# Kernel optimization log

Measured on AMD Instinct MI355X. Metric: run time of the kernel, lower is better.

## Reference

```python
import jax, jax.numpy as jnp
import numpy as np

EPS = 1e-12  # matches torch F.normalize eps

def _l2norm(v, axis):
    n = jnp.sqrt(jnp.sum(v * v, axis=axis, keepdims=True))
    return v / jnp.maximum(n, EPS)

def setup_inputs() -> dict:
    key = jax.random.key(0)
    k1, k2, k3 = jax.random.split(key, 3)
    N, D, H, W, K = 64, 128, 56, 56, 64
    x = jax.random.normal(k1, (N, D, H, W), dtype=jnp.float32)
    conv_w = jax.random.normal(k2, (K, D), dtype=jnp.float32) * 0.05
    centroids = jax.random.uniform(k3, (K, D), dtype=jnp.float32)
    return {"x": x, "conv_w": conv_w, "centroids": centroids}

def reference(x, conv_w, centroids):
    # x: [N, D, H, W]; conv_w: [K, D] (1x1 conv, no bias); centroids: [K, D]
    N, D, H, W = x.shape
    K = centroids.shape[0]
    L = H * W
    # descriptor-wise L2 normalization over channel dim
    x = _l2norm(x, axis=1)
    xf = x.reshape(N, D, L)                      # [N, D, L]
    # 1x1 conv == per-pixel matmul; softmax over clusters
    logits = jnp.einsum('ndl,kd->nkl', xf, conv_w)  # [N, K, L]
    a = jax.nn.softmax(logits, axis=1)              # [N, K, L]
    # vlad[n,k,d] = sum_l a[n,k,l] * (x[n,d,l] - c[k,d])
    #            = (a @ x^T) - (sum_l a) * c   (matmul reformulation)
    vlad = jnp.einsum('nkl,ndl->nkd', a, xf) - a.sum(axis=-1)[:, :, None] * centroids[None]
    # intra-normalize over descriptor dim, flatten, global L2 normalize
    vlad = _l2norm(vlad, axis=2)
    vlad = vlad.reshape(N, K * D)
    vlad = _l2norm(vlad, axis=1)
    return vlad
```

## Files before the change

### kernel.cpp

```cpp
#include <hip/hip_runtime.h>
#include <hip/hip_bf16.h>

#define N_   64
#define D_   128
#define L_   3136
#define K_   64
#define TL_  64
#define NG_  12
#define ASH  72

typedef short  short8  __attribute__((ext_vector_type(8)));
typedef short  short4v __attribute__((ext_vector_type(4)));
typedef float  f32x16  __attribute__((ext_vector_type(16)));

static __device__ __forceinline__ unsigned short f2bf(float f) {
    unsigned u = __float_as_uint(f);
    return (unsigned short)((u + 0x7FFFu + ((u >> 16) & 1u)) >> 16);
}
static __device__ __forceinline__ float bf2f(short s) {
    return __uint_as_float(((unsigned)(unsigned short)s) << 16);
}
static __device__ __forceinline__ unsigned pk2(float lo, float hi) {
    __hip_bfloat162 b = __float22bfloat162_rn(make_float2(lo, hi));
    return *reinterpret_cast<unsigned*>(&b);
}

#define BARX() asm volatile("s_waitcnt lgkmcnt(0)\n\ts_barrier" ::: "memory")

__global__ __launch_bounds__(256, 2)
void vlad_main(const float* __restrict__ x, const float* __restrict__ w,
               float* __restrict__ vout, float* __restrict__ aout,
               int vstride, int astride)
{
    __shared__ __align__(16) short L1[TL_ * D_];
    __shared__ __align__(16) short L2[D_ * TL_];
    __shared__ __align__(16) char  AsRaw[K_ * ASH * 2];
    __shared__ float nrm_lds[TL_];
    __shared__ float dred[4][32];

    const int t    = threadIdx.x;
    const int lane = t & 63;
    const int wv   = __builtin_amdgcn_readfirstlane(t >> 6);
    const int n    = blockIdx.x / NG_;
    const int g    = blockIdx.x % NG_;
    const int tile0 = (g == 0) ? 0 : (4 * g + 1);
    const int ntile = (g == 0) ? 5 : 4;

    const int Mt = wv & 1;
    const int lg = lane >> 5;
    const int lm = lane & 31;

    char* L1b = (char*)L1;
    char* L2b = (char*)L2;
    short* AsS = (short*)AsRaw;
    float (*red_ss)[68] = (float (*)[68])AsRaw;

    short8 wf[8];
#pragma unroll
    for (int ks = 0; ks < 8; ++ks) {
        const float* wp = w + (size_t)(32 * Mt + lm) * D_ + 16 * ks + 8 * lg;
        const float4 wa = *(const float4*)wp;
        const float4 wb = *(const float4*)(wp + 4);
        union { unsigned u[4]; short8 s; } f;
        f.u[0] = pk2(wa.x, wa.y); f.u[1] = pk2(wa.z, wa.w);
        f.u[2] = pk2(wb.x, wb.y); f.u[3] = pk2(wb.z, wb.w);
        wf[ks] = f.s;
    }

    f32x16 acc0 = {0};
    f32x16 acc1 = {0};
    float asum_acc = 0.f;

    const int q  = t >> 4;
    const int l0 = (t & 15) * 4;
    const float* xb = x + (size_t)n * D_ * L_;

    float4 v[8];
    {
        const int p0 = tile0 * TL_;
#pragma unroll
        for (int r = 0; r < 8; ++r)
            v[r] = *(const float4*)(xb + (size_t)(8 * q + r) * L_ + p0 + l0);
    }

    for (int ti = 0; ti < ntile; ++ti) {
#pragma unroll
        for (int j = 0; j < 4; ++j) {
            float s = 0.f;
#pragma unroll
            for (int r = 0; r < 8; ++r) {
                const float val = (&v[r].x)[j];
                s = fmaf(val, val, s);
            }
            red_ss[q][l0 + j] = s;
        }
#pragma unroll
        for (int j = 0; j < 4; ++j) {
            const int l = l0 + j;
            union { unsigned u[4]; short8 s; } f;
            f.u[0] = pk2((&v[0].x)[j], (&v[1].x)[j]);
            f.u[1] = pk2((&v[2].x)[j], (&v[3].x)[j]);
            f.u[2] = pk2((&v[4].x)[j], (&v[5].x)[j]);
            f.u[3] = pk2((&v[6].x)[j], (&v[7].x)[j]);
            *(short8*)(L1b + l * 256 + ((16 * q) ^ ((l & 15) << 4))) = f.s;
        }
#pragma unroll
        for (int r = 0; r < 8; ++r) {
            const int d = 8 * q + r;
            union { unsigned u[2]; short4v s; } f;
            f.u[0] = pk2(v[r].x, v[r].y);
            f.u[1] = pk2(v[r].z, v[r].w);
            *(short4v*)(L2b + d * 128 + ((l0 * 2) ^ ((d & 7) << 4))) = f.s;
        }
        if (ti + 1 < ntile) {
            const int p0n = (tile0 + ti + 1) * TL_;
#pragma unroll
            for (int r = 0; r < 8; ++r)
                v[r] = *(const float4*)(xb + (size_t)(8 * q + r) * L_ + p0n + l0);
        }
        BARX();
        if (t < TL_) {
            float ss = 0.f;
#pragma unroll
            for (int qq = 0; qq < 16; ++qq) ss += red_ss[qq][t];
            nrm_lds[t] = fmaxf(sqrtf(ss), 1e-12f);
        }
        f32x16 r1 = {0};
        {
            const int l = 32 * (wv >> 1) + lm;
            const int rowoff = l * 256;
            const int swz = (l & 15) << 4;
            __builtin_amdgcn_s_setprio(1);
#pragma unroll
            for (int ks = 0; ks < 8; ++ks) {
                const short8 bfr = *(short8*)(L1b + rowoff + (((16 * ks + 8 * lg) * 2) ^ swz));
                r1 = __builtin_amdgcn_mfma_f32_32x32x16_bf16(wf[ks], bfr, r1, 0, 0, 0);
            }
            __builtin_amdgcn_s_setprio(0);
        }
        const int myl = 32 * (wv >> 1) + lm;
        float ss16 = 0.f;
#pragma unroll
        for (int qq = 0; qq < 16; ++qq) ss16 += red_ss[qq][myl];
        const float invp = 1.f / fmaxf(sqrtf(ss16), 1e-12f);
        float e[16];
        float s = 0.f;
#pragma unroll
        for (int r = 0; r < 16; ++r) { e[r] = __expf(r1[r] * invp); s += e[r]; }
        s += __shfl_xor(s, 32);
        if (lane < 32) dred[wv][lm] = s;
        BARX();
        const float denom = dred[wv][lm] + dred[wv ^ 1][lm];
        const float sc = invp / denom;
        {
            const int colp = 32 * (wv >> 1) + lm;
#pragma unroll
            for (int r = 0; r < 16; ++r) {
                const int k = 32 * Mt + (r & 3) + 8 * (r >> 2) + 4 * lg;
                AsS[k * ASH + colp] = (short)f2bf(e[r] * sc);
            }
        }
        BARX();
        {
            short8 af[4];
            const char* arow = AsRaw + (size_t)(32 * Mt + lm) * (ASH * 2);
#pragma unroll
            for (int ks = 0; ks < 4; ++ks)
                af[ks] = *(const short8*)(arow + (16 * ks + 8 * lg) * 2);
            __builtin_amdgcn_s_setprio(1);
#pragma unroll
            for (int nt = 0; nt < 2; ++nt) {
                const int dk = 32 * (2 * (wv >> 1) + nt) + lm;
                const int rowoff = dk * 128;
                const int swz = (dk & 7) << 4;
                f32x16 a = (nt == 0) ? acc0 : acc1;
#pragma unroll
                for (int ks = 0; ks < 4; ++ks) {
                    const short8 bfr = *(short8*)(L2b + rowoff + (((16 * ks + 8 * lg) * 2) ^ swz));
                    a = __builtin_amdgcn_mfma_f32_32x32x16_bf16(af[ks], bfr, a, 0, 0, 0);
                }
                if (nt == 0) acc0 = a; else acc1 = a;
            }
            __builtin_amdgcn_s_setprio(0);
        }
        {
            const int k  = 16 * wv + (lane & 15);
            const int c4 = lane >> 4;
            const char* ap = AsRaw + (size_t)k * (ASH * 2) + c4 * 32;
            const short8 a0 = *(const short8*)ap;
            const short8 a1 = *(const short8*)(ap + 16);
            float ps = 0.f;
#pragma unroll
            for (int i = 0; i < 8; ++i) {
                ps = fmaf(bf2f(a0[i]), nrm_lds[16 * c4 + i],     ps);
                ps = fmaf(bf2f(a1[i]), nrm_lds[16 * c4 + 8 + i], ps);
            }
            ps += __shfl_xor(ps, 16);
            ps += __shfl_xor(ps, 32);
            asum_acc += ps;
        }
        BARX();
    }
    {
        const int dbase0 = 32 * (2 * (wv >> 1));
        float* vb = vstride ? (vout + (size_t)g * vstride) : vout;
#pragma unroll
        for (int r = 0; r < 16; ++r) {
            const int k = 32 * Mt + (r & 3) + 8 * (r >> 2) + 4 * lg;
            float* row = vb + ((size_t)n * K_ + k) * D_ + lm;
            if (vstride) {
                row[dbase0]      = acc0[r];
                row[dbase0 + 32] = acc1[r];
            } else {
                atomicAdd(&row[dbase0],      acc0[r]);
                atomicAdd(&row[dbase0 + 32], acc1[r]);
            }
        }
        if (lane < 16) {
            const int k = 16 * wv + lane;
            if (astride) aout[(size_t)g * astride + n * K_ + k] = asum_acc;
            else atomicAdd(&aout[n * K_ + k], asum_acc);
        }
    }
}

__global__ __launch_bounds__(256)
void vlad_fin(const float* __restrict__ vacc, const float* __restrict__ asum,
              const float* __restrict__ cent, float* __restrict__ out, int npart)
{
    const int t   = threadIdx.x;
    const int b   = blockIdx.x;
    const int n   = b >> 3;
    const int oct = b & 7;
    const int k   = oct * 8 + (t >> 5);
    const int c   = t & 31;

    float a = 0.f;
#pragma unroll 4
    for (int g = 0; g < npart; ++g) a += asum[(size_t)g * (N_ * K_) + n * K_ + k];

    const size_t off4 = ((size_t)(n * K_ + k) * D_ >> 2) + c;
    float4 v = make_float4(0.f, 0.f, 0.f, 0.f);
#pragma unroll 4
    for (int g = 0; g < npart; ++g) {
        const float4 s = ((const float4*)vacc)[(size_t)g * ((size_t)N_ * K_ * D_ >> 2) + off4];
        v.x += s.x; v.y += s.y; v.z += s.z; v.w += s.w;
    }
    const float4 cc = ((const float4*)cent)[((size_t)k * D_ >> 2) + c];
    v.x -= a * cc.x; v.y -= a * cc.y; v.z -= a * cc.z; v.w -= a * cc.w;
    float ss = v.x * v.x + v.y * v.y + v.z * v.z + v.w * v.w;
    ss += __shfl_xor(ss, 1);
    ss += __shfl_xor(ss, 2);
    ss += __shfl_xor(ss, 4);
    ss += __shfl_xor(ss, 8);
    ss += __shfl_xor(ss, 16);
    const float s1 = 0.125f / fmaxf(sqrtf(ss), 1e-12f);
    float4 o;
    o.x = v.x * s1; o.y = v.y * s1; o.z = v.z * s1; o.w = v.w * s1;
    ((float4*)out)[off4] = o;
}

extern "C" void kernel_launch(void* const* d_in, const int* in_sizes, int n_in,
                              void* d_out, int out_size, void* d_ws, size_t ws_size,
                              hipStream_t stream)
{
    const float* x = (const float*)d_in[0];
    const float* w = (const float*)d_in[1];
    const float* c = (const float*)d_in[2];
    float* out = (float*)d_out;

    const size_t vs  = (size_t)N_ * K_ * D_;
    const size_t as_ = (size_t)N_ * K_;
    const size_t need = (NG_ * vs + NG_ * as_) * sizeof(float);
    float* vacc = (float*)d_ws;

    if (ws_size >= need) {
        float* ap = vacc + NG_ * vs;
        vlad_main<<<dim3(N_ * NG_), dim3(256), 0, stream>>>(x, w, vacc, ap,
                                                            (int)vs, (int)as_);
        vlad_fin<<<dim3(N_ * 8), dim3(256), 0, stream>>>(vacc, ap, c, out, NG_);
    } else {
        float* ap = vacc + vs;
        hipMemsetAsync(d_ws, 0, (vs + as_) * sizeof(float), stream);
        vlad_main<<<dim3(N_ * NG_), dim3(256), 0, stream>>>(x, w, vacc, ap, 0, 0);
        vlad_fin<<<dim3(N_ * 8), dim3(256), 0, stream>>>(vacc, ap, c, out, 1);
    }
}
```

Before: 42.47 us.

## Double-buffer x tile prefetch two tiles ahead and use fewer, larger blocks per image

Measured after the change: 38.96 us. -8.3%, faster.

```diff
diff --git a/kernel.cpp b/kernel.cpp
--- a/kernel.cpp
+++ b/kernel.cpp
@@ -6,7 +6,7 @@
 #define L_   3136
 #define K_   64
 #define TL_  64
-#define NG_  12
+#define NG_  8
 #define ASH  72
 
 typedef short  short8  __attribute__((ext_vector_type(8)));
@@ -26,6 +26,132 @@
 }
 
 #define BARX() asm volatile("s_waitcnt lgkmcnt(0)\n\ts_barrier" ::: "memory")
+
+#define PROCESS(VBUF, TCUR, TNEXT)                                             \
+    {                                                                          \
+                                    \
+        _Pragma("unroll")                                                      \
+        for (int j = 0; j < 4; ++j) {                                          \
+            float s = 0.f;                                                     \
+            _Pragma("unroll")                                                  \
+            for (int r = 0; r < 8; ++r) {                                      \
+                const float val = (&VBUF[r].x)[j];                             \
+                s = fmaf(val, val, s);                                         \
+            }                                                                  \
+            red_ss[q][l0 + j] = s;                                             \
+        }                                                                      \
+        _Pragma("unroll")                                                      \
+        for (int j = 0; j < 4; ++j) {                                          \
+            const int l = l0 + j;                                              \
+            union { unsigned u[4]; short8 s; } f;                              \
+            f.u[0] = pk2((&VBUF[0].x)[j], (&VBUF[1].x)[j]);                    \
+            f.u[1] = pk2((&VBUF[2].x)[j], (&VBUF[3].x)[j]);                    \
+            f.u[2] = pk2((&VBUF[4].x)[j], (&VBUF[5].x)[j]);                    \
+            f.u[3] = pk2((&VBUF[6].x)[j], (&VBUF[7].x)[j]);                    \
+            *(short8*)(L1b + l * 256 + ((16 * q) ^ ((l & 15) << 4))) = f.s;    \
+        }                                                                      \
+        _Pragma("unroll")                                                      \
+        for (int r = 0; r < 8; ++r) {                                          \
+            const int d = 8 * q + r;                                           \
+            union { unsigned u[2]; short4v s; } f;                             \
+            f.u[0] = pk2(VBUF[r].x, VBUF[r].y);                                \
+            f.u[1] = pk2(VBUF[r].z, VBUF[r].w);                                \
+            *(short4v*)(L2b + d * 128 + ((l0 * 2) ^ ((d & 7) << 4))) = f.s;    \
+        }                                                                      \
+              \
+        if ((TNEXT) < ntile) {                                                 \
+            const int p0n = (tile0 + (TNEXT)) * TL_;                           \
+            _Pragma("unroll")                                                  \
+            for (int r = 0; r < 8; ++r)                                        \
+                VBUF[r] = *(const float4*)(xb + (size_t)(8 * q + r) * L_ + p0n + l0); \
+        }                                                                      \
+        BARX();                                            \
+        if (t < TL_) {                                                         \
+            float ss = 0.f;                                                    \
+            _Pragma("unroll")                                                  \
+            for (int qq = 0; qq < 16; ++qq) ss += red_ss[qq][t];               \
+            nrm_lds[t] = fmaxf(sqrtf(ss), 1e-12f);                             \
+        }                                                                      \
+                                   \
+        f32x16 r1 = {0};                                                       \
+        {                                                                      \
+            const int l = 32 * (wv >> 1) + lm;                                 \
+            const int rowoff = l * 256;                                        \
+            const int swz = (l & 15) << 4;                                     \
+            __builtin_amdgcn_s_setprio(1);                                     \
+            _Pragma("unroll")                                                  \
+            for (int ks = 0; ks < 8; ++ks) {                                   \
+                const short8 bfr = *(short8*)(L1b + rowoff + (((16 * ks + 8 * lg) * 2) ^ swz)); \
+                r1 = __builtin_amdgcn_mfma_f32_32x32x16_bf16(wf[ks], bfr, r1, 0, 0, 0); \
+            }                                                                  \
+            __builtin_amdgcn_s_setprio(0);                                     \
+        }                                                                      \
+        const int myl = 32 * (wv >> 1) + lm;                                   \
+        float ss16 = 0.f;                                                      \
+        _Pragma("unroll")                                                      \
+        for (int qq = 0; qq < 16; ++qq) ss16 += red_ss[qq][myl];               \
+        const float invp = 1.f / fmaxf(sqrtf(ss16), 1e-12f);                   \
+                \
+        float e[16];                                                           \
+        float s = 0.f;                                                         \
+        _Pragma("unroll")                                                      \
+        for (int r = 0; r < 16; ++r) { e[r] = __expf(r1[r] * invp); s += e[r]; } \
+        s += __shfl_xor(s, 32);                                                \
+        if (lane < 32) dred[wv][lm] = s;                                       \
+        BARX();                            \
+        const float denom = dred[wv][lm] + dred[wv ^ 1][lm];                   \
+        const float sc = invp / denom;                                         \
+        {                                                                      \
+            const int colp = 32 * (wv >> 1) + lm;                              \
+            _Pragma("unroll")                                                  \
+            for (int r = 0; r < 16; ++r) {                                     \
+                const int k = 32 * Mt + (r & 3) + 8 * (r >> 2) + 4 * lg;       \
+                AsS[k * ASH + colp] = (short)f2bf(e[r] * sc);                  \
+            }                                                                  \
+        }                                                                      \
+        BARX();                                              \
+                                \
+        {                                                                      \
+            short8 af[4];                                                      \
+            const char* arow = AsRaw + (size_t)(32 * Mt + lm) * (ASH * 2);     \
+            _Pragma("unroll")                                                  \
+            for (int ks = 0; ks < 4; ++ks)                                     \
+                af[ks] = *(const short8*)(arow + (16 * ks + 8 * lg) * 2);      \
+            __builtin_amdgcn_s_setprio(1);                                     \
+            _Pragma("unroll")                                                  \
+            for (int nt = 0; nt < 2; ++nt) {                                   \
+                const int dk = 32 * (2 * (wv >> 1) + nt) + lm;                 \
+                const int rowoff = dk * 128;                                   \
+                const int swz = (dk & 7) << 4;                                 \
+                f32x16 a = (nt == 0) ? acc0 : acc1;                            \
+                _Pragma("unroll")                                              \
+                for (int ks = 0; ks < 4; ++ks) {                               \
+                    const short8 bfr = *(short8*)(L2b + rowoff + (((16 * ks + 8 * lg) * 2) ^ swz)); \
+                    a = __builtin_amdgcn_mfma_f32_32x32x16_bf16(af[ks], bfr, a, 0, 0, 0); \
+                }                                                              \
+                if (nt == 0) acc0 = a; else acc1 = a;                          \
+            }                                                                  \
+            __builtin_amdgcn_s_setprio(0);                                     \
+        }                                                                      \
+                                                             \
+        {                                                                      \
+            const int k  = 16 * wv + (lane & 15);                              \
+            const int c4 = lane >> 4;                                          \
+            const char* ap = AsRaw + (size_t)k * (ASH * 2) + c4 * 32;          \
+            const short8 a0 = *(const short8*)ap;                              \
+            const short8 a1 = *(const short8*)(ap + 16);                       \
+            float ps = 0.f;                                                    \
+            _Pragma("unroll")                                                  \
+            for (int i = 0; i < 8; ++i) {                                      \
+                ps = fmaf(bf2f(a0[i]), nrm_lds[16 * c4 + i],     ps);          \
+                ps = fmaf(bf2f(a1[i]), nrm_lds[16 * c4 + 8 + i], ps);          \
+            }                                                                  \
+            ps += __shfl_xor(ps, 16);                                          \
+            ps += __shfl_xor(ps, 32);                                          \
+            asum_acc += ps;                                                    \
+        }                                                                      \
+        BARX();                                   \
+    }
 
 __global__ __launch_bounds__(256, 2)
 void vlad_main(const float* __restrict__ x, const float* __restrict__ w,
@@ -43,8 +169,8 @@
     const int wv   = __builtin_amdgcn_readfirstlane(t >> 6);
     const int n    = blockIdx.x / NG_;
     const int g    = blockIdx.x % NG_;
-    const int tile0 = (g == 0) ? 0 : (4 * g + 1);
-    const int ntile = (g == 0) ? 5 : 4;
+    const int tile0 = (g == 0) ? 0 : (7 + 6 * (g - 1));
+    const int ntile = (g == 0) ? 7 : 6;
 
     const int Mt = wv & 1;
     const int lg = lane >> 5;
@@ -75,139 +201,32 @@
     const int l0 = (t & 15) * 4;
     const float* xb = x + (size_t)n * D_ * L_;
 
-    float4 v[8];
+    float4 va[8], vb[8];
     {
         const int p0 = tile0 * TL_;
 #pragma unroll
         for (int r = 0; r < 8; ++r)
-            v[r] = *(const float4*)(xb + (size_t)(8 * q + r) * L_ + p0 + l0);
-    }
-
-    for (int ti = 0; ti < ntile; ++ti) {
+            va[r] = *(const float4*)(xb + (size_t)(8 * q + r) * L_ + p0 + l0);
+        const int p1 = (tile0 + 1) * TL_;
 #pragma unroll
-        for (int j = 0; j < 4; ++j) {
-            float s = 0.f;
-#pragma unroll
-            for (int r = 0; r < 8; ++r) {
-                const float val = (&v[r].x)[j];
-                s = fmaf(val, val, s);
-            }
-            red_ss[q][l0 + j] = s;
+        for (int r = 0; r < 8; ++r)
+            vb[r] = *(const float4*)(xb + (size_t)(8 * q + r) * L_ + p1 + l0);
+    }
+
+    for (int tp = 0; tp < ntile; tp += 2) {
+        PROCESS(va, tp, tp + 2)
+        if (tp + 1 < ntile) {
+            PROCESS(vb, tp + 1, tp + 3)
         }
-#pragma unroll
-        for (int j = 0; j < 4; ++j) {
-            const int l = l0 + j;
-            union { unsigned u[4]; short8 s; } f;
-            f.u[0] = pk2((&v[0].x)[j], (&v[1].x)[j]);
-            f.u[1] = pk2((&v[2].x)[j], (&v[3].x)[j]);
-            f.u[2] = pk2((&v[4].x)[j], (&v[5].x)[j]);
-            f.u[3] = pk2((&v[6].x)[j], (&v[7].x)[j]);
-            *(short8*)(L1b + l * 256 + ((16 * q) ^ ((l & 15) << 4))) = f.s;
-        }
-#pragma unroll
-        for (int r = 0; r < 8; ++r) {
-            const int d = 8 * q + r;
-            union { unsigned u[2]; short4v s; } f;
-            f.u[0] = pk2(v[r].x, v[r].y);
-            f.u[1] = pk2(v[r].z, v[r].w);
-            *(short4v*)(L2b + d * 128 + ((l0 * 2) ^ ((d & 7) << 4))) = f.s;
-        }
-        if (ti + 1 < ntile) {
-            const int p0n = (tile0 + ti + 1) * TL_;
-#pragma unroll
-            for (int r = 0; r < 8; ++r)
-                v[r] = *(const float4*)(xb + (size_t)(8 * q + r) * L_ + p0n + l0);
-        }
-        BARX();
-        if (t < TL_) {
-            float ss = 0.f;
-#pragma unroll
-            for (int qq = 0; qq < 16; ++qq) ss += red_ss[qq][t];
-            nrm_lds[t] = fmaxf(sqrtf(ss), 1e-12f);
-        }
-        f32x16 r1 = {0};
-        {
-            const int l = 32 * (wv >> 1) + lm;
-            const int rowoff = l * 256;
-            const int swz = (l & 15) << 4;
-            __builtin_amdgcn_s_setprio(1);
-#pragma unroll
-            for (int ks = 0; ks < 8; ++ks) {
-                const short8 bfr = *(short8*)(L1b + rowoff + (((16 * ks + 8 * lg) * 2) ^ swz));
-                r1 = __builtin_amdgcn_mfma_f32_32x32x16_bf16(wf[ks], bfr, r1, 0, 0, 0);
-            }
-            __builtin_amdgcn_s_setprio(0);
-        }
-        const int myl = 32 * (wv >> 1) + lm;
-        float ss16 = 0.f;
-#pragma unroll
-        for (int qq = 0; qq < 16; ++qq) ss16 += red_ss[qq][myl];
-        const float invp = 1.f / fmaxf(sqrtf(ss16), 1e-12f);
-        float e[16];
-        float s = 0.f;
-#pragma unroll
-        for (int r = 0; r < 16; ++r) { e[r] = __expf(r1[r] * invp); s += e[r]; }
-        s += __shfl_xor(s, 32);
-        if (lane < 32) dred[wv][lm] = s;
-        BARX();
-        const float denom = dred[wv][lm] + dred[wv ^ 1][lm];
-        const float sc = invp / denom;
-        {
-            const int colp = 32 * (wv >> 1) + lm;
-#pragma unroll
-            for (int r = 0; r < 16; ++r) {
-                const int k = 32 * Mt + (r & 3) + 8 * (r >> 2) + 4 * lg;
-                AsS[k * ASH + colp] = (short)f2bf(e[r] * sc);
-            }
-        }
-        BARX();
-        {
-            short8 af[4];
-            const char* arow = AsRaw + (size_t)(32 * Mt + lm) * (ASH * 2);
-#pragma unroll
-            for (int ks = 0; ks < 4; ++ks)
-                af[ks] = *(const short8*)(arow + (16 * ks + 8 * lg) * 2);
-            __builtin_amdgcn_s_setprio(1);
-#pragma unroll
-            for (int nt = 0; nt < 2; ++nt) {
-                const int dk = 32 * (2 * (wv >> 1) + nt) + lm;
-                const int rowoff = dk * 128;
-                const int swz = (dk & 7) << 4;
-                f32x16 a = (nt == 0) ? acc0 : acc1;
-#pragma unroll
-                for (int ks = 0; ks < 4; ++ks) {
-                    const short8 bfr = *(short8*)(L2b + rowoff + (((16 * ks + 8 * lg) * 2) ^ swz));
-                    a = __builtin_amdgcn_mfma_f32_32x32x16_bf16(af[ks], bfr, a, 0, 0, 0);
-                }
-                if (nt == 0) acc0 = a; else acc1 = a;
-            }
-            __builtin_amdgcn_s_setprio(0);
-        }
-        {
-            const int k  = 16 * wv + (lane & 15);
-            const int c4 = lane >> 4;
-            const char* ap = AsRaw + (size_t)k * (ASH * 2) + c4 * 32;
-            const short8 a0 = *(const short8*)ap;
-            const short8 a1 = *(const short8*)(ap + 16);
-            float ps = 0.f;
-#pragma unroll
-            for (int i = 0; i < 8; ++i) {
-                ps = fmaf(bf2f(a0[i]), nrm_lds[16 * c4 + i],     ps);
-                ps = fmaf(bf2f(a1[i]), nrm_lds[16 * c4 + 8 + i], ps);
-            }
-            ps += __shfl_xor(ps, 16);
-            ps += __shfl_xor(ps, 32);
-            asum_acc += ps;
-        }
-        BARX();
-    }
+    }
+
     {
         const int dbase0 = 32 * (2 * (wv >> 1));
-        float* vb = vstride ? (vout + (size_t)g * vstride) : vout;
+        float* vb2 = vstride ? (vout + (size_t)g * vstride) : vout;
 #pragma unroll
         for (int r = 0; r < 16; ++r) {
             const int k = 32 * Mt + (r & 3) + 8 * (r >> 2) + 4 * lg;
-            float* row = vb + ((size_t)n * K_ + k) * D_ + lm;
+            float* row = vb2 + ((size_t)n * K_ + k) * D_ + lm;
             if (vstride) {
                 row[dbase0]      = acc0[r];
                 row[dbase0 + 32] = acc1[r];
```

## Store bf16 VLAD partials, cut split to 8 groups, shuffle-reduce norms

Applied to the files above, without the earlier changes.

Measured after the change: 35.20 us. 17.1% less time.

```diff
diff --git a/kernel.cpp b/kernel.cpp
--- a/kernel.cpp
+++ b/kernel.cpp
@@ -6,8 +6,9 @@
 #define L_   3136
 #define K_   64
 #define TL_  64
-#define NG_  12
+#define NG_  8
 #define ASH  72
+#define VSLAB ((size_t)N_ * K_ * D_)
 
 typedef short  short8  __attribute__((ext_vector_type(8)));
 typedef short  short4v __attribute__((ext_vector_type(4)));
@@ -29,13 +30,13 @@
 
 __global__ __launch_bounds__(256, 2)
 void vlad_main(const float* __restrict__ x, const float* __restrict__ w,
-               float* __restrict__ vout, float* __restrict__ aout,
-               int vstride, int astride)
+               short* __restrict__ vout, float* __restrict__ aout)
 {
     __shared__ __align__(16) short L1[TL_ * D_];
     __shared__ __align__(16) short L2[D_ * TL_];
     __shared__ __align__(16) char  AsRaw[K_ * ASH * 2];
-    __shared__ float nrm_lds[TL_];
+    __shared__ __align__(16) float red4[4][TL_];
+    __shared__ __align__(16) float nrm_lds[TL_];
     __shared__ float dred[4][32];
 
     const int t    = threadIdx.x;
@@ -43,8 +44,8 @@
     const int wv   = __builtin_amdgcn_readfirstlane(t >> 6);
     const int n    = blockIdx.x / NG_;
     const int g    = blockIdx.x % NG_;
-    const int tile0 = (g == 0) ? 0 : (4 * g + 1);
-    const int ntile = (g == 0) ? 5 : 4;
+    const int tile0 = (g == 0) ? 0 : (7 + 6 * (g - 1));
+    const int ntile = (g == 0) ? 7 : 6;
 
     const int Mt = wv & 1;
     const int lg = lane >> 5;
@@ -53,7 +54,6 @@
     char* L1b = (char*)L1;
     char* L2b = (char*)L2;
     short* AsS = (short*)AsRaw;
-    float (*red_ss)[68] = (float (*)[68])AsRaw;
 
     short8 wf[8];
 #pragma unroll
@@ -84,6 +84,7 @@
     }
 
     for (int ti = 0; ti < ntile; ++ti) {
+        float s4[4];
 #pragma unroll
         for (int j = 0; j < 4; ++j) {
             float s = 0.f;
@@ -92,8 +93,15 @@
                 const float val = (&v[r].x)[j];
                 s = fmaf(val, val, s);
             }
-            red_ss[q][l0 + j] = s;
-        }
+            s4[j] = s;
+        }
+#pragma unroll
+        for (int j = 0; j < 4; ++j) {
+            s4[j] += __shfl_xor(s4[j], 16);
+            s4[j] += __shfl_xor(s4[j], 32);
+        }
+        if (lane < 16)
+            *(float4*)&red4[wv][lane * 4] = make_float4(s4[0], s4[1], s4[2], s4[3]);
 #pragma unroll
         for (int j = 0; j < 4; ++j) {
             const int l = l0 + j;
@@ -120,9 +128,7 @@
         }
         BARX();
         if (t < TL_) {
-            float ss = 0.f;
-#pragma unroll
-            for (int qq = 0; qq < 16; ++qq) ss += red_ss[qq][t];
+            const float ss = red4[0][t] + red4[1][t] + red4[2][t] + red4[3][t];
             nrm_lds[t] = fmaxf(sqrtf(ss), 1e-12f);
         }
         f32x16 r1 = {0};
@@ -139,9 +145,7 @@
             __builtin_amdgcn_s_setprio(0);
         }
         const int myl = 32 * (wv >> 1) + lm;
-        float ss16 = 0.f;
-#pragma unroll
-        for (int qq = 0; qq < 16; ++qq) ss16 += red_ss[qq][myl];
+        const float ss16 = red4[0][myl] + red4[1][myl] + red4[2][myl] + red4[3][myl];
         const float invp = 1.f / fmaxf(sqrtf(ss16), 1e-12f);
         float e[16];
         float s = 0.f;
@@ -155,9 +159,12 @@
         {
             const int colp = 32 * (wv >> 1) + lm;
 #pragma unroll
-            for (int r = 0; r < 16; ++r) {
+            for (int rr = 0; rr < 8; ++rr) {
+                const int r = 2 * rr;
                 const int k = 32 * Mt + (r & 3) + 8 * (r >> 2) + 4 * lg;
-                AsS[k * ASH + colp] = (short)f2bf(e[r] * sc);
+                const unsigned u = pk2(e[r] * sc, e[r + 1] * sc);
+                AsS[k * ASH + colp]       = (short)u;
+                AsS[(k + 1) * ASH + colp] = (short)(u >> 16);
             }
         }
         BARX();
@@ -189,12 +196,17 @@
             const char* ap = AsRaw + (size_t)k * (ASH * 2) + c4 * 32;
             const short8 a0 = *(const short8*)ap;
             const short8 a1 = *(const short8*)(ap + 16);
+            const float4* np = (const float4*)&nrm_lds[16 * c4];
+            const float4 n0 = np[0], n1 = np[1], n2 = np[2], n3 = np[3];
             float ps = 0.f;
-#pragma unroll
-            for (int i = 0; i < 8; ++i) {
-                ps = fmaf(bf2f(a0[i]), nrm_lds[16 * c4 + i],     ps);
-                ps = fmaf(bf2f(a1[i]), nrm_lds[16 * c4 + 8 + i], ps);
-            }
+            ps = fmaf(bf2f(a0[0]), n0.x, ps); ps = fmaf(bf2f(a0[1]), n0.y, ps);
+            ps = fmaf(bf2f(a0[2]), n0.z, ps); ps = fmaf(bf2f(a0[3]), n0.w, ps);
+            ps = fmaf(bf2f(a0[4]), n1.x, ps); ps = fmaf(bf2f(a0[5]), n1.y, ps);
+            ps = fmaf(bf2f(a0[6]), n1.z, ps); ps = fmaf(bf2f(a0[7]), n1.w, ps);
+            ps = fmaf(bf2f(a1[0]), n2.x, ps); ps = fmaf(bf2f(a1[1]), n2.y, ps);
+            ps = fmaf(bf2f(a1[2]), n2.z, ps); ps = fmaf(bf2f(a1[3]), n2.w, ps);
+            ps = fmaf(bf2f(a1[4]), n3.x, ps); ps = fmaf(bf2f(a1[5]), n3.y, ps);
+            ps = fmaf(bf2f(a1[6]), n3.z, ps); ps = fmaf(bf2f(a1[7]), n3.w, ps);
             ps += __shfl_xor(ps, 16);
             ps += __shfl_xor(ps, 32);
             asum_acc += ps;
@@ -203,30 +215,25 @@
     }
     {
         const int dbase0 = 32 * (2 * (wv >> 1));
-        float* vb = vstride ? (vout + (size_t)g * vstride) : vout;
+        short* vb2 = vout + (size_t)g * VSLAB;
 #pragma unroll
         for (int r = 0; r < 16; ++r) {
             const int k = 32 * Mt + (r & 3) + 8 * (r >> 2) + 4 * lg;
-            float* row = vb + ((size_t)n * K_ + k) * D_ + lm;
-            if (vstride) {
-                row[dbase0]      = acc0[r];
-                row[dbase0 + 32] = acc1[r];
-            } else {
-                atomicAdd(&row[dbase0],      acc0[r]);
-                atomicAdd(&row[dbase0 + 32], acc1[r]);
-            }
+            short* row = vb2 + ((size_t)n * K_ + k) * D_ + lm;
+            const unsigned u = pk2(acc0[r], acc1[r]);
+            row[dbase0]      = (short)u;
+            row[dbase0 + 32] = (short)(u >> 16);
         }
         if (lane < 16) {
             const int k = 16 * wv + lane;
-            if (astride) aout[(size_t)g * astride + n * K_ + k] = asum_acc;
-            else atomicAdd(&aout[n * K_ + k], asum_acc);
+            aout[(size_t)g * (N_ * K_) + n * K_ + k] = asum_acc;
         }
     }
 }
 
 __global__ __launch_bounds__(256)
-void vlad_fin(const float* __restrict__ vacc, const float* __restrict__ asum,
-              const float* __restrict__ cent, float* __restrict__ out, int npart)
+void vlad_fin(const short* __restrict__ vacc, const float* __restrict__ asum,
+              const float* __restrict__ cent, float* __restrict__ out)
 {
     const int t   = threadIdx.x;
     const int b   = blockIdx.x;
@@ -236,15 +243,16 @@
     const int c   = t & 31;
 
     float a = 0.f;
-#pragma unroll 4
-    for (int g = 0; g < npart; ++g) a += asum[(size_t)g * (N_ * K_) + n * K_ + k];
-
-    const size_t off4 = ((size_t)(n * K_ + k) * D_ >> 2) + c;
+#pragma unroll
+    for (int g = 0; g < NG_; ++g) a += asum[(size_t)g * (N_ * K_) + n * K_ + k];
+
+    const size_t roff = ((size_t)(n * K_ + k)) * D_ + c * 4;
     float4 v = make_float4(0.f, 0.f, 0.f, 0.f);
-#pragma unroll 4
-    for (int g = 0; g < npart; ++g) {
-        const float4 s = ((const float4*)vacc)[(size_t)g * ((size_t)N_ * K_ * D_ >> 2) + off4];
-        v.x += s.x; v.y += s.y; v.z += s.z; v.w += s.w;
+#pragma unroll
+    for (int g = 0; g < NG_; ++g) {
+        const short4v s = *(const short4v*)(vacc + (size_t)g * VSLAB + roff);
+        v.x += bf2f(s[0]); v.y += bf2f(s[1]);
+        v.z += bf2f(s[2]); v.w += bf2f(s[3]);
     }
     const float4 cc = ((const float4*)cent)[((size_t)k * D_ >> 2) + c];
     v.x -= a * cc.x; v.y -= a * cc.y; v.z -= a * cc.z; v.w -= a * cc.w;
@@ -257,7 +265,7 @@
     const float s1 = 0.125f / fmaxf(sqrtf(ss), 1e-12f);
     float4 o;
     o.x = v.x * s1; o.y = v.y * s1; o.z = v.z * s1; o.w = v.w * s1;
-    ((float4*)out)[off4] = o;
+    *(float4*)(out + roff) = o;
 }
 
 extern "C" void kernel_launch(void* const* d_in, const int* in_sizes, int n_in,
@@ -269,20 +277,9 @@
     const float* c = (const float*)d_in[2];
     float* out = (float*)d_out;
 
-    const size_t vs  = (size_t)N_ * K_ * D_;
-    const size_t as_ = (size_t)N_ * K_;
-    const size_t need = (NG_ * vs + NG_ * as_) * sizeof(float);
-    float* vacc = (float*)d_ws;
-
-    if (ws_size >= need) {
-        float* ap = vacc + NG_ * vs;
-        vlad_main<<<dim3(N_ * NG_), dim3(256), 0, stream>>>(x, w, vacc, ap,
-                                                            (int)vs, (int)as_);
-        vlad_fin<<<dim3(N_ * 8), dim3(256), 0, stream>>>(vacc, ap, c, out, NG_);
-    } else {
-        float* ap = vacc + vs;
-        hipMemsetAsync(d_ws, 0, (vs + as_) * sizeof(float), stream);
-        vlad_main<<<dim3(N_ * NG_), dim3(256), 0, stream>>>(x, w, vacc, ap, 0, 0);
-        vlad_fin<<<dim3(N_ * 8), dim3(256), 0, stream>>>(vacc, ap, c, out, 1);
-    }
-}
+    short* vacc = (short*)d_ws;
+    float* ap   = (float*)(vacc + NG_ * VSLAB);
+
+    vlad_main<<<dim3(N_ * NG_), dim3(256), 0, stream>>>(x, w, vacc, ap);
+    vlad_fin<<<dim3(N_ * 8), dim3(256), 0, stream>>>(vacc, ap, c, out);
+}
```
